# Optimization experiments

Measured on AMD Instinct MI355X. Metric: run time of the kernel, lower is better.

## Reference

```python
import jax, jax.numpy as jnp
import numpy as np

QMIN, QMAX = -128.0, 127.0


def setup_inputs() -> dict:
    key = jax.random.key(0)
    k1, k2, k3 = jax.random.split(key, 3)
    x = jax.random.normal(k1, (8, 32, 32, 32), jnp.float32)          # NCHW
    weight = jax.random.normal(k2, (32, 32, 3, 3), jnp.float32) * 0.1  # OIHW
    bias = jax.random.normal(k3, (32,), jnp.float32) * 0.01
    # lut[i, j] = (i - 128) * (j - 128), indexed by (q + 128).
    i = jnp.arange(256, dtype=jnp.float32) - 128.0
    lut = i[:, None] * i[None, :]
    return {"x": x, "weight": weight, "bias": bias, "lut": lut}


def reference(x, weight, bias, lut):
    # dynamic per-tensor scales (qmethod = ('dynamic','tensor','tensor'))
    sf = jax.lax.stop_gradient(jnp.max(jnp.abs(x)) / 127.0)
    sw = jax.lax.stop_gradient(jnp.max(jnp.abs(weight)) / 127.0)

    qx = jnp.clip(jnp.round(x / sf), QMIN, QMAX)        # int8 values as float
    qw = jnp.clip(jnp.round(weight / sw), QMIN, QMAX)

    # STE fake-quant tensors (forward = dequant, backward = identity)
    x_fq = x + jax.lax.stop_gradient(qx * sf - x)
    w_fq = weight + jax.lax.stop_gradient(qw * sw - weight)

    pad = ((1, 1), (1, 1))
    conv_fq = jax.lax.conv_general_dilated(
        x_fq, w_fq, window_strides=(1, 1), padding=pad,
        dimension_numbers=('NCHW', 'OIHW', 'NCHW'))

    # ---- LUT-based int8 conv path (forward value) ----
    # im2col on the int8 activation codes; zero padding -> q=0 -> index 128,
    # and lut[128, :] == 0, matching zero-padded conv.
    patches = jax.lax.conv_general_dilated_patches(
        qx, filter_shape=(3, 3), window_strides=(1, 1), padding=pad)
    N, K, Hp, Wp = patches.shape                       # K = Cin*kh*kw
    O = qw.shape[0]
    ix = (patches + 128.0).astype(jnp.int32).reshape(N, K, Hp * Wp)
    ix = jnp.transpose(ix, (0, 2, 1))                  # [N, P, K]
    iw = (qw.reshape(O, K) + 128.0).astype(jnp.int32)  # [O, K]

    # gather approximate products and accumulate over the window
    prods = lut[ix[:, :, None, :], iw[None, None, :, :]]  # [N, P, O, K]
    out_lut = (sf * sw) * jnp.sum(prods, axis=-1)          # [N, P, O]
    out_lut = jnp.transpose(out_lut, (0, 2, 1)).reshape(N, O, Hp, Wp)

    b = bias[None, :, None, None]
    out_fq = conv_fq + b
    out_lut = out_lut + b
    # forward returns the LUT result; gradients flow through the fake-quant conv (STE)
    return out_fq + jax.lax.stop_gradient(out_lut - out_fq)
```

## Files before the change

### kernel.cpp

```cpp
#include <hip/hip_runtime.h>

#define W_N 9216

static __device__ __forceinline__ int dot4(int a, int b, int acc) {
#if defined(__has_builtin)
#if __has_builtin(__builtin_amdgcn_sdot4)
  return __builtin_amdgcn_sdot4(a, b, acc, false);
#define DOT4_DONE 1
#endif
#endif
#ifndef DOT4_DONE
  #pragma unroll
  for (int k = 0; k < 4; k++)
    acc += ((a >> (8*k)) << 24 >> 24) * ((b >> (8*k)) << 24 >> 24);
  return acc;
#endif
}

__global__ __launch_bounds__(256) void k_absmax_wq(
    const float4* __restrict__ x4, const float* __restrict__ w,
    float* __restrict__ partials, float* __restrict__ sfsw,
    signed char* __restrict__ qw_r) {
  __shared__ float red[256];
  __shared__ float s_sw;
  int b = blockIdx.x, t = threadIdx.x;

  if (b < 64) {
    float m = 0.f;
    #pragma unroll
    for (int k = 0; k < 4; k++) {
      float4 v = x4[b * 1024 + k * 256 + t];
      m = fmaxf(m, fmaxf(fmaxf(fabsf(v.x), fabsf(v.y)), fmaxf(fabsf(v.z), fabsf(v.w))));
    }
    red[t] = m;
    __syncthreads();
    #pragma unroll
    for (int s = 128; s >= 1; s >>= 1) {
      if (t < s) red[t] = fmaxf(red[t], red[t + s]);
      __syncthreads();
    }
    if (t == 0) partials[b] = red[0];
    return;
  }

  const float4* w4 = (const float4*)w;
  float m = 0.f;
  #pragma unroll
  for (int j = 0; j < 9; j++) {
    float4 v = w4[t + 256 * j];
    m = fmaxf(m, fmaxf(fmaxf(fabsf(v.x), fabsf(v.y)), fmaxf(fabsf(v.z), fabsf(v.w))));
  }
  red[t] = m;
  __syncthreads();
  #pragma unroll
  for (int s = 128; s >= 1; s >>= 1) {
    if (t < s) red[t] = fmaxf(red[t], red[t + s]);
    __syncthreads();
  }
  if (t == 0) { s_sw = red[0] / 127.f; sfsw[1] = s_sw; }
  __syncthreads();
  float sw = s_sw;
  #pragma unroll
  for (int j = 0; j < 36; j++) {
    int i = t + 256 * j;
    int o = i / 288, rem = i % 288;
    int c = rem / 9, k9 = rem % 9;
    float r = rintf(w[i] / sw);
    r = fminf(fmaxf(r, -128.f), 127.f);
    qw_r[(o * 9 + k9) * 32 + c] = (signed char)(int)r;
  }
}

__global__ __launch_bounds__(256) void k_fused(
    const float* __restrict__ x, const float* __restrict__ partials,
    const float* __restrict__ sfsw, const signed char* __restrict__ qw_r,
    const float* __restrict__ bias, float* __restrict__ out) {
  __shared__ float red[64];
  __shared__ float s_sf;
  __shared__ __align__(16) int qxt[4][34][8];

  int b = blockIdx.x, t = threadIdx.x;
  int n = b >> 5, hpair = (b >> 1) & 15, ohalf = b & 1;
  int h0 = hpair * 2;

  int w = t & 31, g = t >> 5;
  float xv[4][4];
  #pragma unroll
  for (int r = 0; r < 4; r++) {
    int y = h0 - 1 + r;
    bool valid = (y >= 0) && (y < 32);
    #pragma unroll
    for (int j = 0; j < 4; j++) {
      int c = g * 4 + j;
      xv[r][j] = valid ? x[n * 32768 + c * 1024 + y * 32 + w] : 0.f;
    }
  }

  if (t < 64) red[t] = partials[t];
  __syncthreads();
  if (t < 32) red[t] = fmaxf(red[t], red[t + 32]);
  __syncthreads();
  if (t < 16) red[t] = fmaxf(red[t], red[t + 16]);
  __syncthreads();
  if (t < 8)  red[t] = fmaxf(red[t], red[t + 8]);
  __syncthreads();
  if (t < 4)  red[t] = fmaxf(red[t], red[t + 4]);
  __syncthreads();
  if (t < 2)  red[t] = fmaxf(red[t], red[t + 2]);
  __syncthreads();
  if (t == 0) s_sf = fmaxf(red[0], red[1]) / 127.f;
  __syncthreads();
  float inv_sf = 1.f / s_sf;

  #pragma unroll
  for (int r = 0; r < 4; r++) {
    int packed = 0;
    #pragma unroll
    for (int j = 0; j < 4; j++) {
      float rr = fminf(fmaxf(rintf(xv[r][j] * inv_sf), -128.f), 127.f);
      packed |= ((int)rr & 0xff) << (8 * j);
    }
    qxt[r][w + 1][g] = packed;
  }
  if (t < 64) {
    int r = t >> 4, col = ((t >> 3) & 1) * 33, g2 = t & 7;
    qxt[r][col][g2] = 0;
  }
  __syncthreads();

  int wv = t >> 6, l = t & 63;
  int hs = l >> 5, ww = l & 31;
  int h = h0 + hs;

  int4 p[3][6];
  #pragma unroll
  for (int r = 0; r < 3; r++) {
    const int4* row = (const int4*)(&qxt[hs + r][ww][0]);
    #pragma unroll
    for (int k = 0; k < 6; k++) p[r][k] = row[k];
  }

  float scale = s_sf * sfsw[1];

  #pragma unroll
  for (int j = 0; j < 4; j++) {
    int o = __builtin_amdgcn_readfirstlane(ohalf * 16 + wv * 4 + j);
    const int* wr = (const int*)qw_r + o * 72;
    int acc = 0;
    #pragma unroll
    for (int ky = 0; ky < 3; ky++) {
      const int* wk = wr + ky * 24;
      #pragma unroll
      for (int k = 0; k < 6; k++) {
        int4 pp = p[ky][k];
        acc = dot4(pp.x, wk[k * 4 + 0], acc);
        acc = dot4(pp.y, wk[k * 4 + 1], acc);
        acc = dot4(pp.z, wk[k * 4 + 2], acc);
        acc = dot4(pp.w, wk[k * 4 + 3], acc);
      }
    }
    out[(n * 32 + o) * 1024 + h * 32 + ww] = scale * (float)acc + bias[o];
  }
}

extern "C" void kernel_launch(void* const* d_in, const int* in_sizes, int n_in,
                              void* d_out, int out_size, void* d_ws, size_t ws_size,
                              hipStream_t stream) {
  (void)in_sizes; (void)n_in; (void)out_size; (void)ws_size;
  const float* x    = (const float*)d_in[0];
  const float* w    = (const float*)d_in[1];
  const float* bias = (const float*)d_in[2];
  float* out = (float*)d_out;

  char* ws = (char*)d_ws;
  float*       partials = (float*)(ws + 0);
  float*       sfsw     = (float*)(ws + 512);
  signed char* qw_r     = (signed char*)(ws + 2048);

  k_absmax_wq<<<65, 256, 0, stream>>>((const float4*)x, w, partials, sfsw, qw_r);
  k_fused<<<256, 256, 0, stream>>>(x, partials, sfsw, qw_r, bias, out);
}
```

Measured before the change: 69.27 us.

## Fuse absmax and conv into one kernel with a grid-wide atomic barrier

Merges the two kernels into one. Each block computes the x absmax over its own halo tile, publishes it with atomicMax, and recomputes the weight absmax and int8 weight quantization into LDS. All 256 blocks then spin on an atomic counter as a grid barrier before quantizing x and running the dot4 conv. This removes the second launch and the global qw round trip. In exchange it adds a memset, redundant per-block weight work, and relies on every block being co-resident, since the spin barrier can deadlock otherwise.

```diff
diff --git a/kernel.cpp b/kernel.cpp
--- a/kernel.cpp
+++ b/kernel.cpp
@@ -1,6 +1,4 @@
 #include <hip/hip_runtime.h>
-
-#define W_N 9216
 
 static __device__ __forceinline__ int dot4(int a, int b, int acc) {
 #if defined(__has_builtin)
@@ -17,49 +15,62 @@
 #endif
 }
 
-__global__ __launch_bounds__(256) void k_absmax_wq(
-    const float4* __restrict__ x4, const float* __restrict__ w,
-    float* __restrict__ partials, float* __restrict__ sfsw,
-    signed char* __restrict__ qw_r) {
+__global__ __launch_bounds__(256) void k_all(
+    const float* __restrict__ x, const float* __restrict__ w,
+    const float* __restrict__ bias, float* __restrict__ out,
+    unsigned* __restrict__ sync) {
   __shared__ float red[256];
-  __shared__ float s_sw;
+  __shared__ float s_sf, s_sw;
+  __shared__ __align__(16) int qw_lds[2304];
+  __shared__ __align__(16) int qxt[4][34][8];
+
   int b = blockIdx.x, t = threadIdx.x;
+  int n = b >> 5, hpair = (b >> 1) & 15, ohalf = b & 1;
+  int h0 = hpair * 2;
 
-  if (b < 64) {
-    float m = 0.f;
+  int wlane = t & 31, g = t >> 5;
+  float xv[4][4];
+  float mx = 0.f;
+  #pragma unroll
+  for (int r = 0; r < 4; r++) {
+    int y = h0 - 1 + r;
+    bool valid = (y >= 0) && (y < 32);
     #pragma unroll
-    for (int k = 0; k < 4; k++) {
-      float4 v = x4[b * 1024 + k * 256 + t];
-      m = fmaxf(m, fmaxf(fmaxf(fabsf(v.x), fabsf(v.y)), fmaxf(fabsf(v.z), fabsf(v.w))));
+    for (int j = 0; j < 4; j++) {
+      float vv = valid ? x[n * 32768 + (g * 4 + j) * 1024 + y * 32 + wlane] : 0.f;
+      xv[r][j] = vv;
+      mx = fmaxf(mx, fabsf(vv));
     }
-    red[t] = m;
-    __syncthreads();
-    #pragma unroll
-    for (int s = 128; s >= 1; s >>= 1) {
-      if (t < s) red[t] = fmaxf(red[t], red[t + s]);
-      __syncthreads();
-    }
-    if (t == 0) partials[b] = red[0];
-    return;
   }
 
-  const float4* w4 = (const float4*)w;
-  float m = 0.f;
-  #pragma unroll
-  for (int j = 0; j < 9; j++) {
-    float4 v = w4[t + 256 * j];
-    m = fmaxf(m, fmaxf(fmaxf(fabsf(v.x), fabsf(v.y)), fmaxf(fabsf(v.z), fabsf(v.w))));
-  }
-  red[t] = m;
+  red[t] = mx;
   __syncthreads();
   #pragma unroll
   for (int s = 128; s >= 1; s >>= 1) {
     if (t < s) red[t] = fmaxf(red[t], red[t + s]);
     __syncthreads();
   }
-  if (t == 0) { s_sw = red[0] / 127.f; sfsw[1] = s_sw; }
+  if (t == 0) atomicMax(&sync[0], __float_as_uint(red[0]));
+  __syncthreads();
+
+  float mw = 0.f;
+  #pragma unroll
+  for (int j = 0; j < 9; j++) {
+    float4 u = ((const float4*)w)[t + 256 * j];
+    mw = fmaxf(mw, fmaxf(fmaxf(fabsf(u.x), fabsf(u.y)), fmaxf(fabsf(u.z), fabsf(u.w))));
+  }
+  red[t] = mw;
+  __syncthreads();
+  #pragma unroll
+  for (int s = 128; s >= 1; s >>= 1) {
+    if (t < s) red[t] = fmaxf(red[t], red[t + s]);
+    __syncthreads();
+  }
+  if (t == 0) s_sw = red[0] / 127.f;
   __syncthreads();
   float sw = s_sw;
+
+  signed char* qw8 = (signed char*)qw_lds;
   #pragma unroll
   for (int j = 0; j < 36; j++) {
     int i = t + 256 * j;
@@ -67,48 +78,18 @@
     int c = rem / 9, k9 = rem % 9;
     float r = rintf(w[i] / sw);
     r = fminf(fmaxf(r, -128.f), 127.f);
-    qw_r[(o * 9 + k9) * 32 + c] = (signed char)(int)r;
-  }
-}
-
-__global__ __launch_bounds__(256) void k_fused(
-    const float* __restrict__ x, const float* __restrict__ partials,
-    const float* __restrict__ sfsw, const signed char* __restrict__ qw_r,
-    const float* __restrict__ bias, float* __restrict__ out) {
-  __shared__ float red[64];
-  __shared__ float s_sf;
-  __shared__ __align__(16) int qxt[4][34][8];
-
-  int b = blockIdx.x, t = threadIdx.x;
-  int n = b >> 5, hpair = (b >> 1) & 15, ohalf = b & 1;
-  int h0 = hpair * 2;
-
-  int w = t & 31, g = t >> 5;
-  float xv[4][4];
-  #pragma unroll
-  for (int r = 0; r < 4; r++) {
-    int y = h0 - 1 + r;
-    bool valid = (y >= 0) && (y < 32);
-    #pragma unroll
-    for (int j = 0; j < 4; j++) {
-      int c = g * 4 + j;
-      xv[r][j] = valid ? x[n * 32768 + c * 1024 + y * 32 + w] : 0.f;
-    }
+    qw8[(o * 9 + k9) * 32 + c] = (signed char)(int)r;
   }
 
-  if (t < 64) red[t] = partials[t];
-  __syncthreads();
-  if (t < 32) red[t] = fmaxf(red[t], red[t + 32]);
-  __syncthreads();
-  if (t < 16) red[t] = fmaxf(red[t], red[t + 16]);
-  __syncthreads();
-  if (t < 8)  red[t] = fmaxf(red[t], red[t + 8]);
-  __syncthreads();
-  if (t < 4)  red[t] = fmaxf(red[t], red[t + 4]);
-  __syncthreads();
-  if (t < 2)  red[t] = fmaxf(red[t], red[t + 2]);
-  __syncthreads();
-  if (t == 0) s_sf = fmaxf(red[0], red[1]) / 127.f;
+  if (t == 0) {
+    __threadfence();
+    atomicAdd(&sync[1], 1u);
+    while (__hip_atomic_load(&sync[1], __ATOMIC_ACQUIRE,
+                             __HIP_MEMORY_SCOPE_AGENT) < 256u)
+      __builtin_amdgcn_s_sleep(2);
+    s_sf = __uint_as_float(__hip_atomic_load(&sync[0], __ATOMIC_RELAXED,
+                                             __HIP_MEMORY_SCOPE_AGENT)) / 127.f;
+  }
   __syncthreads();
   float inv_sf = 1.f / s_sf;
 
@@ -120,7 +101,7 @@
       float rr = fminf(fmaxf(rintf(xv[r][j] * inv_sf), -128.f), 127.f);
       packed |= ((int)rr & 0xff) << (8 * j);
     }
-    qxt[r][w + 1][g] = packed;
+    qxt[r][wlane + 1][g] = packed;
   }
   if (t < 64) {
     int r = t >> 4, col = ((t >> 3) & 1) * 33, g2 = t & 7;
@@ -140,19 +121,19 @@
     for (int k = 0; k < 6; k++) p[r][k] = row[k];
   }
 
-  float scale = s_sf * sfsw[1];
+  float scale = s_sf * sw;
 
   #pragma unroll
   for (int j = 0; j < 4; j++) {
-    int o = __builtin_amdgcn_readfirstlane(ohalf * 16 + wv * 4 + j);
-    const int* wr = (const int*)qw_r + o * 72;
+    int o = ohalf * 16 + wv * 4 + j;
+    const int* wr = qw_lds + o * 72;
     int acc = 0;
     #pragma unroll
     for (int ky = 0; ky < 3; ky++) {
       const int* wk = wr + ky * 24;
       #pragma unroll
       for (int k = 0; k < 6; k++) {
-        int4 pp = p[ky][k];
+        const int4 pp = p[ky][k];
         acc = dot4(pp.x, wk[k * 4 + 0], acc);
         acc = dot4(pp.y, wk[k * 4 + 1], acc);
         acc = dot4(pp.z, wk[k * 4 + 2], acc);
@@ -172,11 +153,7 @@
   const float* bias = (const float*)d_in[2];
   float* out = (float*)d_out;
 
-  char* ws = (char*)d_ws;
-  float*       partials = (float*)(ws + 0);
-  float*       sfsw     = (float*)(ws + 512);
-  signed char* qw_r     = (signed char*)(ws + 2048);
-
-  k_absmax_wq<<<65, 256, 0, stream>>>((const float4*)x, w, partials, sfsw, qw_r);
-  k_fused<<<256, 256, 0, stream>>>(x, partials, sfsw, qw_r, bias, out);
+  unsigned* sync = (unsigned*)d_ws;
+  hipMemsetAsync(d_ws, 0, 8, stream);
+  k_all<<<256, 256, 0, stream>>>(x, w, bias, out, sync);
 }
```

After: 85.61 us. 23.6% more time.
